# Kernel optimization log

Measured on AMD Instinct MI355X. Metric: run time of the kernel, lower is better.

The kernel has to match this reference:

```python
import jax, jax.numpy as jnp
import numpy as np

MAXU = 6          # init arg maxU
MAXV = 6          # init arg maxV (ratio=None)
TRUNC = 4         # cfg.TRUNCATED_SIZE; cfg.TRUNCATED=True, cfg.FLOW_REG_BY_MAX=True


def setup_inputs() -> dict:
    key = jax.random.key(0)
    B, H, W = 8, 128, 160
    U, V = 2 * MAXU + 1, 2 * MAXV + 1
    x = jax.random.normal(key, (B, 1, U, V, H, W), dtype=jnp.float32)
    return {"x": x}


def reference(x):
    # x: [B,1,U,V,H,W] cost volume
    x = x[:, 0]                                   # [B,U,V,H,W]
    b, u, v, h, w = x.shape

    # --- truncation mask (cfg.TRUNCATED) ---
    # argmax over flattened (u,v); scatter one-hot + MaxPool3d((2t+1,2t+1,1))
    # is equivalent to a +-t box around the per-pixel argmax location.
    idx = jnp.argmax(x.reshape(b, u * v, h, w), axis=1)   # [B,H,W] int
    ui = (idx // v)[:, None, None]                        # [B,1,1,H,W]
    vi = (idx % v)[:, None, None]
    ugrid = jnp.arange(u).reshape(1, u, 1, 1, 1)
    vgrid = jnp.arange(v).reshape(1, 1, v, 1, 1)
    mask = (jnp.abs(ugrid - ui) <= TRUNC) & (jnp.abs(vgrid - vi) <= TRUNC)
    xm = jnp.where(mask, x, -jnp.inf)

    # --- softmax over the U*V displacement hypotheses (FLOW_REG_BY_MAX) ---
    p = jax.nn.softmax(xm.reshape(b, u * v, h, w), axis=1).reshape(b, u, v, h, w)

    dispU = jnp.arange(-MAXU, MAXU + 1, dtype=x.dtype)    # [U]
    dispV = jnp.arange(-MAXV, MAXV + 1, dtype=x.dtype)    # [V]
    flowU = jnp.einsum('buvhw,u->bhw', p, dispU)
    flowV = jnp.einsum('buvhw,v->bhw', p, dispV)
    return jnp.stack((flowU, flowV), axis=1)              # [B,2,H,W]
```

## Files before the change

### kernel.cpp

```cpp
#include <hip/hip_runtime.h>
#include <math.h>

#define Bsz 8
#define Udim 13
#define Vdim 13
#define Hdim 128
#define Wdim 160
#define HW (Hdim * Wdim)
#define UV (Udim * Vdim)
#define TRUNC 4
#define NPIX (Bsz * HW)

__global__ __launch_bounds__(256) void flow_regression_kernel(
    const float* __restrict__ x, float* __restrict__ out) {
    int p = blockIdx.x * 256 + threadIdx.x;
    if (p >= NPIX) return;
    int b  = p / HW;
    int hw = p - b * HW;

    const float* base = x + (size_t)b * UV * HW + hw;

    float m = -INFINITY;
    int mi = 0;
    {
        const float* q = base;
        #pragma unroll 13
        for (int i = 0; i < UV; ++i) {
            float v = *q;
            q += HW;
            if (v > m) { m = v; mi = i; }
        }
    }
    int ui = mi / Vdim;
    int vi = mi - ui * Vdim;

    float sum = 0.f, wu = 0.f, wv = 0.f;
    {
        const float* q = base;
        for (int u = 0; u < Udim; ++u) {
            bool uin = (u - ui <= TRUNC) && (ui - u <= TRUNC);
            float du = (float)(u - 6);
            #pragma unroll
            for (int v = 0; v < Vdim; ++v) {
                float val = *q;
                q += HW;
                bool in = uin && (v - vi <= TRUNC) && (vi - v <= TRUNC);
                float e = in ? __expf(val - m) : 0.f;
                sum += e;
                wu  += e * du;
                wv  += e * (float)(v - 6);
            }
        }
    }
    float inv = 1.0f / sum;
    float* ob = out + (size_t)b * 2 * HW + hw;
    ob[0]  = wu * inv;
    ob[HW] = wv * inv;
}

extern "C" void kernel_launch(void* const* d_in, const int* in_sizes, int n_in,
                              void* d_out, int out_size, void* d_ws, size_t ws_size,
                              hipStream_t stream) {
    const float* x = (const float*)d_in[0];
    float* out = (float*)d_out;
    int nblocks = (NPIX + 255) / 256;
    flow_regression_kernel<<<nblocks, 256, 0, stream>>>(x, out);
}
```

Measured before the change: 170.1 us.

## Load cost volume once into registers and reuse for argmax and softmax

All 169 cost values per pixel are loaded into a register array in one pass, so the second global-memory read pass is removed and HBM traffic is roughly halved. The argmax and the masked softmax-regression both run over the registers, and the u-dimension mask is applied per row sum rather than per element. Launch bounds now request 2 blocks per CU and the bounds check is dropped because NPIX divides by 256. The large register array may raise register pressure, lowering occupancy or causing spills.

```diff
diff --git a/kernel.cpp b/kernel.cpp
--- a/kernel.cpp
+++ b/kernel.cpp
@@ -11,45 +11,46 @@
 #define TRUNC 4
 #define NPIX (Bsz * HW)
 
-__global__ __launch_bounds__(256) void flow_regression_kernel(
+__global__ __launch_bounds__(256, 2) void flow_regression_kernel(
     const float* __restrict__ x, float* __restrict__ out) {
     int p = blockIdx.x * 256 + threadIdx.x;
-    if (p >= NPIX) return;
     int b  = p / HW;
     int hw = p - b * HW;
 
     const float* base = x + (size_t)b * UV * HW + hw;
 
-    float m = -INFINITY;
+    float vals[UV];
+    #pragma unroll
+    for (int i = 0; i < UV; ++i) {
+        vals[i] = base[(size_t)i * HW];
+    }
+
+    float m = vals[0];
     int mi = 0;
-    {
-        const float* q = base;
-        #pragma unroll 13
-        for (int i = 0; i < UV; ++i) {
-            float v = *q;
-            q += HW;
-            if (v > m) { m = v; mi = i; }
-        }
+    #pragma unroll
+    for (int i = 1; i < UV; ++i) {
+        if (vals[i] > m) { m = vals[i]; mi = i; }
     }
     int ui = mi / Vdim;
     int vi = mi - ui * Vdim;
 
     float sum = 0.f, wu = 0.f, wv = 0.f;
-    {
-        const float* q = base;
-        for (int u = 0; u < Udim; ++u) {
-            bool uin = (u - ui <= TRUNC) && (ui - u <= TRUNC);
-            float du = (float)(u - 6);
-            #pragma unroll
-            for (int v = 0; v < Vdim; ++v) {
-                float val = *q;
-                q += HW;
-                bool in = uin && (v - vi <= TRUNC) && (vi - v <= TRUNC);
-                float e = in ? __expf(val - m) : 0.f;
-                sum += e;
-                wu  += e * du;
-                wv  += e * (float)(v - 6);
-            }
+    #pragma unroll
+    for (int u = 0; u < Udim; ++u) {
+        bool uin = (u - ui <= TRUNC) && (ui - u <= TRUNC);
+        float rsum = 0.f, rwv = 0.f;
+        #pragma unroll
+        for (int v = 0; v < Vdim; ++v) {
+            float val = vals[u * Vdim + v];
+            bool vin = (v - vi <= TRUNC) && (vi - v <= TRUNC);
+            float e = vin ? __expf(val - m) : 0.f;
+            rsum += e;
+            rwv  += e * (float)(v - 6);
+        }
+        if (uin) {
+            sum += rsum;
+            wu  += rsum * (float)(u - 6);
+            wv  += rwv;
         }
     }
     float inv = 1.0f / sum;
@@ -63,6 +64,5 @@
                               hipStream_t stream) {
     const float* x = (const float*)d_in[0];
     float* out = (float*)d_out;
-    int nblocks = (NPIX + 255) / 256;
-    flow_regression_kernel<<<nblocks, 256, 0, stream>>>(x, out);
+    flow_regression_kernel<<<NPIX / 256, 256, 0, stream>>>(x, out);
 }
```

Result: faster. 158.3 us (-6.9%).
